# Performance work log

Hardware: AMD Instinct MI355X
Metric: run time of the kernel (lower is better)

## Reference

```python
import jax, jax.numpy as jnp
import numpy as np
from jax import lax

B, C, O, K, KS, H, W = 16, 256, 256, 4, 3, 64, 64
PAD = 1
BN_EPS = 1e-3


def setup_inputs() -> dict:
    key = jax.random.key(0)
    k1, k2, k3 = jax.random.split(key, 3)
    x = jax.random.normal(k1, (B, C, H, W), dtype=jnp.float32)
    # nn.Parameter(torch.randn(...)) -> standard normal init
    dyn_kernels = jax.random.normal(k2, (K, O, C, KS, KS), dtype=jnp.float32)
    # attention 1x1 conv (no bias): weight [K, C, 1, 1] -> store as [K, C]
    attn_w = jax.random.normal(k3, (K, C), dtype=jnp.float32) / np.sqrt(C).astype(np.float32)
    gamma = jnp.ones((O,), dtype=jnp.float32)
    beta = jnp.zeros((O,), dtype=jnp.float32)
    return {"x": x, "dyn_kernels": dyn_kernels, "attn_w": attn_w, "gamma": gamma, "beta": beta}


def reference(x, dyn_kernels, attn_w, gamma, beta):
    b, c, h, w = x.shape
    k, o = dyn_kernels.shape[0], dyn_kernels.shape[1]
    # attention: global avg pool -> 1x1 conv (no bias) -> softmax over kernels
    pooled = x.mean(axis=(2, 3))                      # [B, C]
    attn = jax.nn.softmax(pooled @ attn_w.T, axis=1)  # [B, K]
    # run all K kernels as a single conv with K*O output channels
    kern = dyn_kernels.reshape(k * o, c, KS, KS)
    y = lax.conv_general_dilated(
        x, kern, window_strides=(1, 1), padding=((PAD, PAD), (PAD, PAD)),
        dimension_numbers=("NCHW", "OIHW", "NCHW"))   # [B, K*O, H, W]
    y = y.reshape(b, k, o, h, w)
    out = jnp.einsum("bkohw,bk->bohw", y, attn)        # weighted sum over kernels
    # BatchNorm2d (training mode: batch statistics, biased variance)
    mean = out.mean(axis=(0, 2, 3))
    var = out.var(axis=(0, 2, 3))
    inv = gamma * lax.rsqrt(var + BN_EPS)
    out = (out - mean[None, :, None, None]) * inv[None, :, None, None] + beta[None, :, None, None]
    # SiLU
    return out * jax.nn.sigmoid(out)
```

## Files before the change

### kernel.cpp

```cpp
#include <hip/hip_runtime.h>
#include <math.h>


#define B_ 16
#define C_ 256
#define O_ 256
#define HW_ 4096
#define PLANE_F4 1024
#define WPERK 589824
#define XS_PX 40

typedef short bf16x8 __attribute__((ext_vector_type(8)));
typedef float f32x16 __attribute__((ext_vector_type(16)));

__device__ __forceinline__ unsigned short f2bf(float f) {
    unsigned u = __float_as_uint(f);
    u += 0x7FFFu + ((u >> 16) & 1u);
    return (unsigned short)(u >> 16);
}
__device__ __forceinline__ float bf2f(unsigned short h) {
    return __uint_as_float((unsigned)h << 16);
}

__global__ __launch_bounds__(256) void pool_kernel(const float4* __restrict__ x4,
                                                   float* __restrict__ pooled) {
    int bc = blockIdx.x;
    const float4* p = x4 + (size_t)bc * PLANE_F4;
    float s = 0.f;
    for (int i = threadIdx.x; i < PLANE_F4; i += 256) {
        float4 v = p[i];
        s += v.x + v.y + v.z + v.w;
    }
    for (int off = 32; off; off >>= 1) s += __shfl_down(s, off);
    __shared__ float partial[4];
    if ((threadIdx.x & 63) == 0) partial[threadIdx.x >> 6] = s;
    __syncthreads();
    if (threadIdx.x == 0)
        pooled[bc] = (partial[0] + partial[1] + partial[2] + partial[3]) * (1.f / 4096.f);
}

__global__ void attn_kernel(const float* __restrict__ pooled,
                            const float* __restrict__ attn_w,
                            float* __restrict__ attn) {
    int tid = threadIdx.x;
    int b = tid >> 2, k = tid & 3;
    float s = 0.f;
    for (int c = 0; c < C_; ++c) s += pooled[b * C_ + c] * attn_w[k * C_ + c];
    __shared__ float lg[16][4];
    lg[b][k] = s;
    __syncthreads();
    float m = fmaxf(fmaxf(lg[b][0], lg[b][1]), fmaxf(lg[b][2], lg[b][3]));
    float den = expf(lg[b][0] - m) + expf(lg[b][1] - m) +
                expf(lg[b][2] - m) + expf(lg[b][3] - m);
    attn[tid] = expf(s - m) / den;
}

__global__ __launch_bounds__(256) void wtrans_kernel(const float* __restrict__ dyn,
                                                     const float* __restrict__ attn,
                                                     unsigned short* __restrict__ wt_hi,
                                                     unsigned short* __restrict__ wt_lo) {
    int idx = blockIdx.x * 256 + threadIdx.x;
    int b = idx >> 16;
    int o = (idx >> 8) & 255;
    int c = idx & 255;
    float a0 = attn[b * 4 + 0], a1 = attn[b * 4 + 1],
          a2 = attn[b * 4 + 2], a3 = attn[b * 4 + 3];
    const float* p0 = dyn + ((size_t)o * 256 + c) * 9;
    float v[9];
#pragma unroll
    for (int t = 0; t < 9; ++t)
        v[t] = a0 * p0[t] + a1 * p0[WPERK + t] + a2 * p0[2 * WPERK + t] + a3 * p0[3 * WPERK + t];
    size_t obase = ((size_t)(b * 256 + o) * 9) * 256 + c;
#pragma unroll
    for (int t = 0; t < 9; ++t) {
        float f = v[t];
        unsigned short h = f2bf(f);
        unsigned short l = f2bf(f - bf2f(h));
        wt_hi[obase + (size_t)t * 256] = h;
        wt_lo[obase + (size_t)t * 256] = l;
    }
}

template <bool FUSED_STATS>
__global__ __launch_bounds__(256, 2) void conv_mfma_kernel(const float* __restrict__ x,
        const unsigned short* __restrict__ wt_hi,
        const unsigned short* __restrict__ wt_lo,
        float* __restrict__ out,
        float* __restrict__ psum,
        float* __restrict__ psumsq) {
    __shared__ __align__(16) unsigned short xs_hi[3 * 66 * XS_PX];
    __shared__ __align__(16) unsigned short xs_lo[3 * 66 * XS_PX];

    const int bid = blockIdx.x;
    const int wk  = (bid & 7) * 128 + (bid >> 3);
    const int b   = wk >> 6;
    const int h   = wk & 63;

    const int tid  = threadIdx.x;
    const int lane = tid & 63;
    const int wid  = tid >> 6;
    const int l31  = lane & 31;
    const int g2   = lane >> 5;
    const int wo   = wid * 64;

    const int sr = tid / 66;
    const int sw = tid - sr * 66;
    const bool sactive = tid < 198;
    const int hh = h - 1 + sr;
    const int ww = sw - 1;
    const bool svalid = sactive && (unsigned)hh < 64u && (unsigned)ww < 64u;
    const float* xsrc = x + (size_t)b * (C_ * HW_) + (size_t)(svalid ? hh : 0) * 64 + (svalid ? ww : 0);
    unsigned short* sh_hi = &xs_hi[(sr * 66 + sw) * XS_PX];
    unsigned short* sh_lo = &xs_lo[(sr * 66 + sw) * XS_PX];

    f32x16 acc[2][2];
#pragma unroll
    for (int i = 0; i < 2; ++i)
#pragma unroll
        for (int j = 0; j < 2; ++j) acc[i][j] = (f32x16)(0.f);

    const unsigned short* wbh = wt_hi + ((size_t)(b * 256 + wo + l31) * 9) * 256 + g2 * 8;
    const unsigned short* wbl = wt_lo + ((size_t)(b * 256 + wo + l31) * 9) * 256 + g2 * 8;
    const unsigned short* xph = xs_hi + l31 * XS_PX + g2 * 8;
    const unsigned short* xpl = xs_lo + l31 * XS_PX + g2 * 8;

#define LOADX(buf, cb) do {                                              \
        if (svalid) {                                                    \
            const float* _p = xsrc + (size_t)(cb) * HW_;                 \
            _Pragma("unroll")                                            \
            for (int _c = 0; _c < 32; ++_c) buf[_c] = _p[(size_t)_c * HW_]; \
        } else {                                                         \
            _Pragma("unroll")                                            \
            for (int _c = 0; _c < 32; ++_c) buf[_c] = 0.f;               \
        }                                                                \
    } while (0)

#define STOREX(buf) do {                                                 \
        if (sactive) {                                                   \
            unsigned _hw[16], _lw[16];                                   \
            _Pragma("unroll")                                            \
            for (int _c = 0; _c < 16; ++_c) {                            \
                unsigned short h0_ = f2bf(buf[2 * _c]);                  \
                unsigned short l0_ = f2bf(buf[2 * _c] - bf2f(h0_));      \
                unsigned short h1_ = f2bf(buf[2 * _c + 1]);              \
                unsigned short l1_ = f2bf(buf[2 * _c + 1] - bf2f(h1_));  \
                _hw[_c] = (unsigned)h0_ | ((unsigned)h1_ << 16);         \
                _lw[_c] = (unsigned)l0_ | ((unsigned)l1_ << 16);         \
            }                                                            \
            _Pragma("unroll")                                            \
            for (int _u = 0; _u < 4; ++_u) {                             \
                *(uint4*)&sh_hi[_u * 8] = make_uint4(_hw[4*_u], _hw[4*_u+1], _hw[4*_u+2], _hw[4*_u+3]); \
                *(uint4*)&sh_lo[_u * 8] = make_uint4(_lw[4*_u], _lw[4*_u+1], _lw[4*_u+2], _lw[4*_u+3]); \
            }                                                            \
        }                                                                \
    } while (0)

#define MFMA_CHUNK(cb) do {                                              \
        _Pragma("unroll")                                                \
        for (int t = 0; t < 9; ++t) {                                    \
            const int dh = t / 3, dw = t % 3;                            \
            bf16x8 bh_[2][2], bl_[2][2];                                 \
            _Pragma("unroll")                                            \
            for (int ks = 0; ks < 2; ++ks)                               \
                _Pragma("unroll")                                        \
                for (int nf = 0; nf < 2; ++nf) {                         \
                    const int xoff = (dh * 66 + dw + nf * 32) * XS_PX + ks * 16; \
                    bh_[ks][nf] = *(const bf16x8*)&xph[xoff];            \
                    bl_[ks][nf] = *(const bf16x8*)&xpl[xoff];            \
                }                                                        \
            bf16x8 ah_[2][2], al_[2][2];                                 \
            _Pragma("unroll")                                            \
            for (int mf = 0; mf < 2; ++mf)                               \
                _Pragma("unroll")                                        \
                for (int ks = 0; ks < 2; ++ks) {                         \
                    const size_t woff = (size_t)mf * 73728 + (size_t)t * 256 + ks * 16 + (cb); \
                    ah_[mf][ks] = *(const bf16x8*)(wbh + woff);          \
                    al_[mf][ks] = *(const bf16x8*)(wbl + woff);          \
                }                                                        \
            __builtin_amdgcn_s_setprio(1);                               \
            _Pragma("unroll")                                            \
            for (int ks = 0; ks < 2; ++ks)                               \
                _Pragma("unroll")                                        \
                for (int mf = 0; mf < 2; ++mf)                           \
                    _Pragma("unroll")                                    \
                    for (int nf = 0; nf < 2; ++nf)                       \
                        acc[mf][nf] = __builtin_amdgcn_mfma_f32_32x32x16_bf16(ah_[mf][ks], bh_[ks][nf], acc[mf][nf], 0, 0, 0); \
            _Pragma("unroll")                                            \
            for (int ks = 0; ks < 2; ++ks)                               \
                _Pragma("unroll")                                        \
                for (int mf = 0; mf < 2; ++mf)                           \
                    _Pragma("unroll")                                    \
                    for (int nf = 0; nf < 2; ++nf)                       \
                        acc[mf][nf] = __builtin_amdgcn_mfma_f32_32x32x16_bf16(ah_[mf][ks], bl_[ks][nf], acc[mf][nf], 0, 0, 0); \
            _Pragma("unroll")                                            \
            for (int ks = 0; ks < 2; ++ks)                               \
                _Pragma("unroll")                                        \
                for (int mf = 0; mf < 2; ++mf)                           \
                    _Pragma("unroll")                                    \
                    for (int nf = 0; nf < 2; ++nf)                       \
                        acc[mf][nf] = __builtin_amdgcn_mfma_f32_32x32x16_bf16(al_[mf][ks], bh_[ks][nf], acc[mf][nf], 0, 0, 0); \
            __builtin_amdgcn_s_setprio(0);                               \
        }                                                                \
    } while (0)

    float xa[32], xb2[32];
    LOADX(xa, 0);
#pragma unroll 1
    for (int cc = 0; cc < 256; cc += 64) {
        __syncthreads();
        STOREX(xa);
        __syncthreads();
        LOADX(xb2, cc + 32);
        MFMA_CHUNK(cc);
        __syncthreads();
        STOREX(xb2);
        __syncthreads();
        if (cc + 64 < 256) LOADX(xa, cc + 64);
        MFMA_CHUNK(cc + 32);
    }

    float* op = out + ((size_t)b * 256 + wo) * HW_ + (size_t)h * 64;
#pragma unroll
    for (int mf = 0; mf < 2; ++mf)
#pragma unroll
        for (int nf = 0; nf < 2; ++nf) {
            f32x16 a = acc[mf][nf];
#pragma unroll
            for (int r = 0; r < 16; ++r) {
                int row = (r & 3) + 8 * (r >> 2) + 4 * g2;
                op[(size_t)(mf * 32 + row) * HW_ + nf * 32 + l31] = a[r];
            }
        }

    if (FUSED_STATS) {
#pragma unroll
        for (int mf = 0; mf < 2; ++mf)
#pragma unroll
            for (int r = 0; r < 16; ++r) {
                float v0 = acc[mf][0][r], v1 = acc[mf][1][r];
                float s = v0 + v1;
                float q = v0 * v0 + v1 * v1;
#pragma unroll
                for (int off = 1; off < 32; off <<= 1) {
                    s += __shfl_xor(s, off);
                    q += __shfl_xor(q, off);
                }
                if (l31 == 0) {
                    int o = wo + mf * 32 + (r & 3) + 8 * (r >> 2) + 4 * g2;
                    psum[(size_t)o * 1024 + wk] = s;
                    psumsq[(size_t)o * 1024 + wk] = q;
                }
            }
    }
#undef LOADX
#undef STOREX
#undef MFMA_CHUNK
}

__global__ __launch_bounds__(256, 2) void conv_otf_kernel(const float* __restrict__ x,
                                                          const float* __restrict__ wsrc,
                                                          const float* __restrict__ attn,
                                                          float* __restrict__ out) {
    __shared__ __align__(16) float xs[8][3][72];
    __shared__ __align__(16) float wsh[64 * 100];
    const int h   = blockIdx.x;
    const int ob  = blockIdx.y * 64;
    const int b   = blockIdx.z;
    const int tid = threadIdx.x;
    const int o_idx = tid >> 4;
    const int w0    = (tid & 15) * 4;
    float a0 = attn[b * 4 + 0], a1 = attn[b * 4 + 1],
          a2 = attn[b * 4 + 2], a3 = attn[b * 4 + 3];
    const float* xb = x + (size_t)b * (C_ * HW_);
    const float* wb = wsrc + (size_t)ob * 2304;
    float acc[4][4];
#pragma unroll
    for (int i = 0; i < 4; ++i)
#pragma unroll
        for (int j = 0; j < 4; ++j) acc[i][j] = 0.f;
    for (int cb = 0; cb < C_; cb += 8) {
        __syncthreads();
        for (int idx = tid; idx < 8 * 3 * 66; idx += 256) {
            int c = idx / 198, rem = idx - c * 198;
            int r = rem / 66, wi = rem - r * 66;
            int hhh = h - 1 + r, ww = wi - 1;
            float v = 0.f;
            if ((unsigned)hhh < 64u && (unsigned)ww < 64u)
                v = xb[(size_t)(cb + c) * HW_ + hhh * 64 + ww];
            xs[c][r][wi] = v;
        }
        for (int idx = tid; idx < 64 * 72; idx += 256) {
            int o = idx / 72, j = idx - o * 72;
            int c = j / 9, t = j - c * 9;
            size_t gi = (size_t)o * 2304 + (size_t)(cb + c) * 9 + t;
            float v = a0 * wb[gi] + a1 * wb[WPERK + gi] +
                      a2 * wb[2 * WPERK + gi] + a3 * wb[3 * WPERK + gi];
            wsh[o * 100 + c * 12 + t] = v;
        }
        __syncthreads();
#pragma unroll
        for (int cc = 0; cc < 8; ++cc) {
            float xr[3][6];
#pragma unroll
            for (int r = 0; r < 3; ++r) {
                float4 a = *(const float4*)&xs[cc][r][w0];
                float2 b2 = *(const float2*)&xs[cc][r][w0 + 4];
                xr[r][0] = a.x; xr[r][1] = a.y; xr[r][2] = a.z; xr[r][3] = a.w;
                xr[r][4] = b2.x; xr[r][5] = b2.y;
            }
#pragma unroll
            for (int oo = 0; oo < 4; ++oo) {
                const float* wp = &wsh[(o_idx * 4 + oo) * 100 + cc * 12];
                float4 wA = *(const float4*)wp;
                float4 wB = *(const float4*)(wp + 4);
                float w8 = wp[8];
#pragma unroll
                for (int ww = 0; ww < 4; ++ww) {
                    acc[oo][ww] += wA.x * xr[0][ww]     + wA.y * xr[0][ww + 1] + wA.z * xr[0][ww + 2]
                                 + wA.w * xr[1][ww]     + wB.x * xr[1][ww + 1] + wB.y * xr[1][ww + 2]
                                 + wB.z * xr[2][ww]     + wB.w * xr[2][ww + 1] + w8   * xr[2][ww + 2];
                }
            }
        }
    }
    float* op = out + ((size_t)b * O_ + ob) * HW_ + h * 64;
#pragma unroll
    for (int oo = 0; oo < 4; ++oo) {
        float4 v = make_float4(acc[oo][0], acc[oo][1], acc[oo][2], acc[oo][3]);
        *(float4*)&op[(size_t)(o_idx * 4 + oo) * HW_ + w0] = v;
    }
}

__global__ __launch_bounds__(256) void stats_full_kernel(const float4* __restrict__ out4,
                                                         const float* __restrict__ gamma,
                                                         float* __restrict__ mean,
                                                         float* __restrict__ inv) {
    int o = blockIdx.x;
    float s = 0.f, s2 = 0.f;
    for (int b = 0; b < B_; ++b) {
        const float4* p = out4 + ((size_t)b * O_ + o) * PLANE_F4;
        for (int i = threadIdx.x; i < PLANE_F4; i += 256) {
            float4 v = p[i];
            s  += v.x + v.y + v.z + v.w;
            s2 += v.x * v.x + v.y * v.y + v.z * v.z + v.w * v.w;
        }
    }
    for (int off = 32; off; off >>= 1) {
        s  += __shfl_down(s, off);
        s2 += __shfl_down(s2, off);
    }
    __shared__ float ps[4], ps2[4];
    int w = threadIdx.x >> 6;
    if ((threadIdx.x & 63) == 0) { ps[w] = s; ps2[w] = s2; }
    __syncthreads();
    if (threadIdx.x == 0) {
        float S = ps[0] + ps[1] + ps[2] + ps[3];
        float S2 = ps2[0] + ps2[1] + ps2[2] + ps2[3];
        float m = S * (1.f / 65536.f);
        float var = S2 * (1.f / 65536.f) - m * m;
        mean[o] = m;
        inv[o] = gamma[o] * rsqrtf(var + 1e-3f);
    }
}

__global__ __launch_bounds__(256) void stats_reduce_kernel(const float* __restrict__ psum,
                                                           const float* __restrict__ psumsq,
                                                           const float* __restrict__ gamma,
                                                           float* __restrict__ mean,
                                                           float* __restrict__ inv) {
    int o = blockIdx.x;
    const float* ps = psum + (size_t)o * 1024;
    const float* pq = psumsq + (size_t)o * 1024;
    float s = 0.f, q = 0.f;
    for (int i = threadIdx.x; i < 1024; i += 256) { s += ps[i]; q += pq[i]; }
    for (int off = 32; off; off >>= 1) {
        s += __shfl_down(s, off);
        q += __shfl_down(q, off);
    }
    __shared__ float a[4], b2[4];
    int w = threadIdx.x >> 6;
    if ((threadIdx.x & 63) == 0) { a[w] = s; b2[w] = q; }
    __syncthreads();
    if (threadIdx.x == 0) {
        float S = a[0] + a[1] + a[2] + a[3];
        float Q = b2[0] + b2[1] + b2[2] + b2[3];
        float m = S * (1.f / 65536.f);
        float var = Q * (1.f / 65536.f) - m * m;
        mean[o] = m;
        inv[o] = gamma[o] * rsqrtf(var + 1e-3f);
    }
}

__global__ __launch_bounds__(256) void bn_silu_kernel(float4* __restrict__ out4,
                                                      const float* __restrict__ mean,
                                                      const float* __restrict__ inv,
                                                      const float* __restrict__ beta) {
    const int total = B_ * O_ * PLANE_F4;
    for (int i = blockIdx.x * 256 + threadIdx.x; i < total; i += gridDim.x * 256) {
        int plane = i >> 10;
        int o = plane & 255;
        float m = mean[o], iv = inv[o], bt = beta[o];
        float4 v = out4[i];
        float u;
        u = (v.x - m) * iv + bt; v.x = u / (1.f + expf(-u));
        u = (v.y - m) * iv + bt; v.y = u / (1.f + expf(-u));
        u = (v.z - m) * iv + bt; v.z = u / (1.f + expf(-u));
        u = (v.w - m) * iv + bt; v.w = u / (1.f + expf(-u));
        out4[i] = v;
    }
}

extern "C" void kernel_launch(void* const* d_in, const int* in_sizes, int n_in,
                              void* d_out, int out_size, void* d_ws, size_t ws_size,
                              hipStream_t stream) {
    const float* x      = (const float*)d_in[0];
    const float* dyn    = (const float*)d_in[1];
    const float* attn_w = (const float*)d_in[2];
    const float* gamma  = (const float*)d_in[3];
    const float* beta   = (const float*)d_in[4];
    float* out = (float*)d_out;
    float* ws  = (float*)d_ws;

    float* pooled = ws;
    float* attn   = ws + 4096;
    float* mean   = ws + 4160;
    float* inv    = ws + 4416;
    unsigned short* wt_hi = (unsigned short*)(ws + 4672);
    unsigned short* wt_lo = wt_hi + 9437184;
    float* psum   = (float*)(wt_lo + 9437184);
    float* psumsq = psum + 262144;

    const size_t need_mfma  = (size_t)4672 * 4 + 2ull * 9437184ull * 2ull;
    const size_t need_fused = need_mfma + 2ull * 262144ull * 4ull;
    const bool mfma_path = ws_size >= need_mfma;
    const bool fused     = ws_size >= need_fused;

    pool_kernel<<<4096, 256, 0, stream>>>((const float4*)x, pooled);
    attn_kernel<<<1, 64, 0, stream>>>(pooled, attn_w, attn);
    if (mfma_path) {
        wtrans_kernel<<<4096, 256, 0, stream>>>(dyn, attn, wt_hi, wt_lo);
        if (fused) {
            conv_mfma_kernel<true><<<1024, 256, 0, stream>>>(x, wt_hi, wt_lo, out, psum, psumsq);
            stats_reduce_kernel<<<256, 256, 0, stream>>>(psum, psumsq, gamma, mean, inv);
        } else {
            conv_mfma_kernel<false><<<1024, 256, 0, stream>>>(x, wt_hi, wt_lo, out, psum, psumsq);
            stats_full_kernel<<<256, 256, 0, stream>>>((const float4*)out, gamma, mean, inv);
        }
    } else {
        conv_otf_kernel<<<dim3(64, 4, 16), 256, 0, stream>>>(x, dyn, attn, out);
        stats_full_kernel<<<256, 256, 0, stream>>>((const float4*)out, gamma, mean, inv);
    }
    bn_silu_kernel<<<4096, 256, 0, stream>>>((float4*)out, mean, inv, beta);
}
```

Measured before the change: 462.0 us.

## Retile weight layout for coalesced MFMA loads and raise occupancy

The per-batch blended weights are now stored as [b][tap][c/16][o][16], so the 16-channel fragments that adjacent lanes (adjacent output channels) read sit next to each other instead of 4.6 KB apart. The conv loop drops the second staging register buffer, loading the next 32-channel chunk into the same buffer. Launch bounds move to 3 blocks per SM. Fewer live registers should allow the higher occupancy, at the cost of less overlap between global loads and MFMA work.

```diff
diff --git a/kernel.cpp b/kernel.cpp
--- a/kernel.cpp
+++ b/kernel.cpp
@@ -70,19 +70,19 @@
 #pragma unroll
     for (int t = 0; t < 9; ++t)
         v[t] = a0 * p0[t] + a1 * p0[WPERK + t] + a2 * p0[2 * WPERK + t] + a3 * p0[3 * WPERK + t];
-    size_t obase = ((size_t)(b * 256 + o) * 9) * 256 + c;
 #pragma unroll
     for (int t = 0; t < 9; ++t) {
         float f = v[t];
         unsigned short h = f2bf(f);
         unsigned short l = f2bf(f - bf2f(h));
-        wt_hi[obase + (size_t)t * 256] = h;
-        wt_lo[obase + (size_t)t * 256] = l;
+        size_t widx = (((size_t)(b * 9 + t) * 16 + (c >> 4)) * 256 + o) * 16 + (c & 15);
+        wt_hi[widx] = h;
+        wt_lo[widx] = l;
     }
 }
 
 template <bool FUSED_STATS>
-__global__ __launch_bounds__(256, 2) void conv_mfma_kernel(const float* __restrict__ x,
+__global__ __launch_bounds__(256, 3) void conv_mfma_kernel(const float* __restrict__ x,
         const unsigned short* __restrict__ wt_hi,
         const unsigned short* __restrict__ wt_lo,
         float* __restrict__ out,
@@ -119,8 +119,8 @@
 #pragma unroll
         for (int j = 0; j < 2; ++j) acc[i][j] = (f32x16)(0.f);
 
-    const unsigned short* wbh = wt_hi + ((size_t)(b * 256 + wo + l31) * 9) * 256 + g2 * 8;
-    const unsigned short* wbl = wt_lo + ((size_t)(b * 256 + wo + l31) * 9) * 256 + g2 * 8;
+    const unsigned short* wbh = wt_hi + (size_t)b * 589824 + (wo + l31) * 16 + g2 * 8;
+    const unsigned short* wbl = wt_lo + (size_t)b * 589824 + (wo + l31) * 16 + g2 * 8;
     const unsigned short* xph = xs_hi + l31 * XS_PX + g2 * 8;
     const unsigned short* xpl = xs_lo + l31 * XS_PX + g2 * 8;
 
@@ -137,20 +137,22 @@
 
 #define STOREX(buf) do {                                                 \
         if (sactive) {                                                   \
-            unsigned _hw[16], _lw[16];                                   \
-            _Pragma("unroll")                                            \
-            for (int _c = 0; _c < 16; ++_c) {                            \
-                unsigned short h0_ = f2bf(buf[2 * _c]);                  \
-                unsigned short l0_ = f2bf(buf[2 * _c] - bf2f(h0_));      \
-                unsigned short h1_ = f2bf(buf[2 * _c + 1]);              \
-                unsigned short l1_ = f2bf(buf[2 * _c + 1] - bf2f(h1_));  \
-                _hw[_c] = (unsigned)h0_ | ((unsigned)h1_ << 16);         \
-                _lw[_c] = (unsigned)l0_ | ((unsigned)l1_ << 16);         \
-            }                                                            \
             _Pragma("unroll")                                            \
             for (int _u = 0; _u < 4; ++_u) {                             \
-                *(uint4*)&sh_hi[_u * 8] = make_uint4(_hw[4*_u], _hw[4*_u+1], _hw[4*_u+2], _hw[4*_u+3]); \
-                *(uint4*)&sh_lo[_u * 8] = make_uint4(_lw[4*_u], _lw[4*_u+1], _lw[4*_u+2], _lw[4*_u+3]); \
+                unsigned _hw[4], _lw[4];                                 \
+                _Pragma("unroll")                                        \
+                for (int _c = 0; _c < 4; ++_c) {                         \
+                    float _f0 = buf[_u * 8 + 2 * _c];                    \
+                    float _f1 = buf[_u * 8 + 2 * _c + 1];                \
+                    unsigned short h0_ = f2bf(_f0);                      \
+                    unsigned short l0_ = f2bf(_f0 - bf2f(h0_));          \
+                    unsigned short h1_ = f2bf(_f1);                      \
+                    unsigned short l1_ = f2bf(_f1 - bf2f(h1_));          \
+                    _hw[_c] = (unsigned)h0_ | ((unsigned)h1_ << 16);     \
+                    _lw[_c] = (unsigned)l0_ | ((unsigned)l1_ << 16);     \
+                }                                                        \
+                *(uint4*)&sh_hi[_u * 8] = make_uint4(_hw[0], _hw[1], _hw[2], _hw[3]); \
+                *(uint4*)&sh_lo[_u * 8] = make_uint4(_lw[0], _lw[1], _lw[2], _lw[3]); \
             }                                                            \
         }                                                                \
     } while (0)
@@ -173,7 +175,8 @@
             for (int mf = 0; mf < 2; ++mf)                               \
                 _Pragma("unroll")                                        \
                 for (int ks = 0; ks < 2; ++ks) {                         \
-                    const size_t woff = (size_t)mf * 73728 + (size_t)t * 256 + ks * 16 + (cb); \
+                    const size_t woff = (size_t)t * 65536 +              \
+                        (size_t)(((cb) >> 4) + ks) * 4096 + mf * 512;    \
                     ah_[mf][ks] = *(const bf16x8*)(wbh + woff);          \
                     al_[mf][ks] = *(const bf16x8*)(wbl + woff);          \
                 }                                                        \
@@ -203,20 +206,15 @@
         }                                                                \
     } while (0)
 
-    float xa[32], xb2[32];
+    float xa[32];
     LOADX(xa, 0);
 #pragma unroll 1
-    for (int cc = 0; cc < 256; cc += 64) {
+    for (int cc = 0; cc < 256; cc += 32) {
         __syncthreads();
         STOREX(xa);
         __syncthreads();
-        LOADX(xb2, cc + 32);
+        if (cc + 32 < 256) LOADX(xa, cc + 32);
         MFMA_CHUNK(cc);
-        __syncthreads();
-        STOREX(xb2);
-        __syncthreads();
-        if (cc + 64 < 256) LOADX(xa, cc + 64);
-        MFMA_CHUNK(cc + 32);
     }
 
     float* op = out + ((size_t)b * 256 + wo) * HW_ + (size_t)h * 64;
```

Result: faster. 415.8 us (-10.0%).
